# Kernel tuning notes

Hardware: AMD Instinct MI355X
Metric: run time of the kernel (lower is better)

The kernel has to match this reference:

```python
import jax, jax.numpy as jnp
import numpy as np

NUM_HEADS = 16
NUM_KV_HEADS = 4
HEAD_DIM = 128
SCALE = 0.08838834764831845  # 1/sqrt(128)
BATCH = 4
SEQLEN = 1024
TOTAL = BATCH * SEQLEN


def setup_inputs() -> dict:
    key = jax.random.key(0)
    kq, kk, kv = jax.random.split(key, 3)
    q = jax.random.normal(kq, (TOTAL, NUM_HEADS, HEAD_DIM), dtype=jnp.float32)
    k = jax.random.normal(kk, (TOTAL, NUM_KV_HEADS, HEAD_DIM), dtype=jnp.float32)
    v = jax.random.normal(kv, (TOTAL, NUM_KV_HEADS, HEAD_DIM), dtype=jnp.float32)
    cu = jnp.arange(BATCH + 1, dtype=jnp.int32) * SEQLEN  # [0,1024,2048,3072,4096]
    return {"q": q, "k": k, "v": v, "cu_seqlens_q": cu, "cu_seqlens_k": cu}


def reference(q, k, v, cu_seqlens_q, cu_seqlens_k):
    # Prefill varlen causal attention (block_tables=None, empty kv cache).
    # Equal-length segments -> reshape packed tokens to [B, S, H, D].
    B = cu_seqlens_q.shape[0] - 1
    S = q.shape[0] // B
    H, Dh = q.shape[1], q.shape[2]
    Hkv = k.shape[1]
    g = H // Hkv  # GQA group size

    qb = q.reshape(B, S, H, Dh)
    # repeat_interleave kv heads to match query heads
    kb = jnp.repeat(k.reshape(B, S, Hkv, Dh), g, axis=2)  # [B,S,H,Dh]
    vb = jnp.repeat(v.reshape(B, S, Hkv, Dh), g, axis=2)

    scores = jnp.einsum('bqhd,bkhd->bhqk', qb, kb) * SCALE  # [B,H,S,S]
    causal = jnp.tril(jnp.ones((S, S), dtype=bool))
    scores = jnp.where(causal, scores, jnp.finfo(scores.dtype).min)
    probs = jax.nn.softmax(scores, axis=-1)
    o = jnp.einsum('bhqk,bkhd->bqhd', probs, vb)  # [B,S,H,Dh]
    return o.reshape(B * S, H, Dh)
```

## Files before the change

kernel.cpp:

```cpp
#include <hip/hip_runtime.h>
#include <cstddef>

#define NH 16
#define NKV 4
#define HD 128
#define SEQ 1024
#define SCALE_F 0.08838834764831845f

typedef __attribute__((ext_vector_type(8))) short short8;
typedef __attribute__((ext_vector_type(4))) float floatx4;

union F8 { short8 v; unsigned short u[8]; };

__device__ __forceinline__ unsigned short f2bf(float f) {
  unsigned int u = __float_as_uint(f);
  u += 0x7FFFu + ((u >> 16) & 1u);
  return (unsigned short)(u >> 16);
}

__device__ __forceinline__ void glds16(const void* g, void* l) {
  __builtin_amdgcn_global_load_lds(
      (const __attribute__((address_space(1))) unsigned int*)g,
      (__attribute__((address_space(3))) unsigned int*)l, 16, 0, 0);
}

__global__ __launch_bounds__(256) void prepass(const float* __restrict__ kg,
                                               const float* __restrict__ vg,
                                               unsigned short* __restrict__ Ktg,
                                               unsigned short* __restrict__ Vtg) {
  __shared__ float Vl[32 * 132];
  const int tid = threadIdx.x;
  const int bid = blockIdx.x;
  if (bid < 512) {
    const int bkvh = bid >> 5, tile = bid & 31;
    const int b = bkvh >> 2, kvh = bkvh & 3;
    const int kpos = tid >> 3;
    const int d8base = (tid & 7) * 2;
    const size_t tok = (size_t)b * SEQ + tile * 32 + kpos;
    const float* src = kg + (tok * NKV + kvh) * HD + d8base * 8;
    unsigned short* dstT = Ktg + (size_t)bid * 4096;
#pragma unroll
    for (int i = 0; i < 2; ++i) {
      floatx4 a = ((const floatx4*)src)[0];
      floatx4 c = ((const floatx4*)src)[1];
      F8 t;
#pragma unroll
      for (int j = 0; j < 4; ++j) { t.u[j] = f2bf(a[j]); t.u[4 + j] = f2bf(c[j]); }
      const int blk = kpos * 16 + ((d8base + i) ^ (kpos & 15));
      *(short8*)(dstT + blk * 8) = t.v;
      src += 8;
    }
  } else {
    const int bb = bid - 512;
    const int bkvh = bb >> 5, tile = bb & 31;
    const int b = bkvh >> 2, kvh = bkvh & 3;
    const int r = tid >> 3;
    const int c16 = (tid & 7) * 16;
    const size_t tok = (size_t)b * SEQ + tile * 32 + r;
    const float* src = vg + (tok * NKV + kvh) * HD + c16;
#pragma unroll
    for (int j = 0; j < 4; ++j)
      *(floatx4*)&Vl[r * 132 + c16 + j * 4] = ((const floatx4*)src)[j];
    __syncthreads();
    unsigned short* dstT = Vtg + (size_t)bb * 4096;
#pragma unroll
    for (int i = 0; i < 2; ++i) {
      const int o = tid * 2 + i;
      const int d = o >> 2, s8 = o & 3;
      F8 t;
#pragma unroll
      for (int j = 0; j < 8; ++j) {
        const int s = s8 * 8 + j;
        const int k = (s >> 1) + ((s & 1) << 4);
        t.u[j] = f2bf(Vl[k * 132 + d]);
      }
      const int blk = d * 4 + (s8 ^ (d & 3));
      *(short8*)(dstT + blk * 8) = t.v;
    }
  }
}

__global__ __launch_bounds__(256, 4)
void fa_fwd2(const float* __restrict__ qg, const unsigned short* __restrict__ Ktg,
             const unsigned short* __restrict__ Vtg, float* __restrict__ og) {
  __shared__ __align__(16) unsigned short Kb[2][4096];
  __shared__ __align__(16) unsigned short Vb[2][4096];
  __shared__ __align__(16) unsigned int Pb[4][16 * 20];

  const int tid = threadIdx.x;
  const int wave = tid >> 6;
  const int lane = tid & 63;
  const int col = lane & 15;
  const int quad = lane >> 4;

  const int idx = blockIdx.x;
  const int g = idx >> 8;
  const int u = (idx >> 6) & 3;
  const int bh = idx & 63;
  const int qt = g * 4 + ((u + g) & 3);
  const int h = bh & 15;
  const int b = bh >> 4;
  const int kvh = h >> 2;
  const int seg = b * SEQ;
  const int wq0 = qt * 64 + wave * 16;
  const int tb = (b * NKV + kvh) * 32;

  F8 qf[4];
  {
    const float* qp = qg + ((size_t)(seg + wq0 + col) * NH + h) * HD + quad * 8;
#pragma unroll
    for (int ks = 0; ks < 4; ++ks) {
      floatx4 a = ((const floatx4*)(qp + ks * 32))[0];
      floatx4 c = ((const floatx4*)(qp + ks * 32))[1];
#pragma unroll
      for (int j = 0; j < 4; ++j) {
        qf[ks].u[j] = f2bf(a[j] * SCALE_F);
        qf[ks].u[4 + j] = f2bf(c[j] * SCALE_F);
      }
    }
  }

  floatx4 acc[8];
#pragma unroll
  for (int dt = 0; dt < 8; ++dt) acc[dt] = (floatx4){0.f, 0.f, 0.f, 0.f};
  float lsum[4] = {0.f, 0.f, 0.f, 0.f};

  const int nkt = 2 * (qt + 1);
  const int stoff = wave * 2048 + lane * 16;

  {
    const char* gK = (const char*)Ktg + (size_t)tb * 8192 + stoff;
    char* lK = (char*)&Kb[0][0] + wave * 2048;
    glds16(gK, lK);
    glds16(gK + 1024, lK + 1024);
    const char* gV = (const char*)Vtg + (size_t)tb * 8192 + stoff;
    char* lV = (char*)&Vb[0][0] + wave * 2048;
    glds16(gV, lV);
    glds16(gV + 1024, lV + 1024);
  }
  __syncthreads();

  for (int kt = 0; kt < nkt; ++kt) {
    const int cb = kt & 1, nb = cb ^ 1;
    if (kt + 1 < nkt) {
      const char* gK = (const char*)Ktg + (size_t)(tb + kt + 1) * 8192 + stoff;
      char* lK = (char*)&Kb[nb][0] + wave * 2048;
      glds16(gK, lK);
      glds16(gK + 1024, lK + 1024);
      const char* gV = (const char*)Vtg + (size_t)(tb + kt + 1) * 8192 + stoff;
      char* lV = (char*)&Vb[nb][0] + wave * 2048;
      glds16(gV, lV);
      glds16(gV + 1024, lV + 1024);
    }
    const int kbase = kt * 32;
    if (kbase <= wq0 + 15) {
      floatx4 s0 = {0.f, 0.f, 0.f, 0.f}, s1 = {0.f, 0.f, 0.f, 0.f};
#pragma unroll
      for (int ks = 0; ks < 4; ++ks) {
        F8 k0, k1;
        k0.v = *(const short8*)&Kb[cb][(col * 16 + ((ks * 4 + quad) ^ col)) * 8];
        k1.v = *(const short8*)&Kb[cb][((16 + col) * 16 + ((ks * 4 + quad) ^ col)) * 8];
        s0 = __builtin_amdgcn_mfma_f32_16x16x32_bf16(qf[ks].v, k0.v, s0, 0, 0, 0);
        s1 = __builtin_amdgcn_mfma_f32_16x16x32_bf16(qf[ks].v, k1.v, s1, 0, 0, 0);
      }
      const bool diag = (kbase + 31 > wq0);
#pragma unroll
      for (int r = 0; r < 4; ++r) {
        float p0 = __expf(s0[r]);
        float p1 = __expf(s1[r]);
        if (diag) {
          const int q0 = wq0 + quad * 4 + r;
          p0 = (kbase + col > q0) ? 0.f : p0;
          p1 = (kbase + 16 + col > q0) ? 0.f : p1;
        }
        lsum[r] += p0 + p1;
        Pb[wave][(quad * 4 + r) * 20 + col] =
            (unsigned int)f2bf(p0) | ((unsigned int)f2bf(p1) << 16);
      }
      F8 pa;
      pa.v = *(const short8*)&Pb[wave][col * 20 + quad * 4];
#pragma unroll
      for (int dt = 0; dt < 8; ++dt) {
        F8 vb;
        vb.v = *(const short8*)&Vb[cb][((dt * 16 + col) * 4 + (quad ^ (col & 3))) * 8];
        acc[dt] = __builtin_amdgcn_mfma_f32_16x16x32_bf16(pa.v, vb.v, acc[dt], 0, 0, 0);
      }
    }
    __syncthreads();
  }

#pragma unroll
  for (int r = 0; r < 4; ++r) {
    float l = lsum[r];
    l += __shfl_xor(l, 1);
    l += __shfl_xor(l, 2);
    l += __shfl_xor(l, 4);
    l += __shfl_xor(l, 8);
    const float inv = 1.0f / l;
    float* op = og + ((size_t)(seg + wq0 + quad * 4 + r) * NH + h) * HD;
#pragma unroll
    for (int dt = 0; dt < 8; ++dt) op[dt * 16 + col] = acc[dt][r] * inv;
  }
}

#define KST 136
#define VST 40
#define PST 40

__global__ __launch_bounds__(256, 2)
void fa_fwd(const float* __restrict__ qg, const float* __restrict__ kg,
            const float* __restrict__ vg, float* __restrict__ og) {
  __shared__ unsigned short Klds[32 * KST];
  __shared__ unsigned short Vt[HD * VST];
  __shared__ unsigned short Pl[4][32 * PST];

  const int tid = threadIdx.x;
  const int wave = tid >> 6;
  const int lane = tid & 63;
  const int col = lane & 15;
  const int quad = lane >> 4;

  const int idx = blockIdx.x;
  const int raw = idx & 7;
  const int qt = (idx & 256) ? raw : 7 - raw;
  const int bh = idx >> 3;
  const int h = bh & 15;
  const int b = bh >> 4;
  const int kvh = h >> 2;
  const int seg = b * SEQ;
  const int wq0 = qt * 128 + wave * 32;

  F8 qf[2][4];
#pragma unroll
  for (int mt = 0; mt < 2; ++mt) {
    const size_t qrow = (size_t)(seg + wq0 + mt * 16 + col);
    const float* qp = qg + (qrow * NH + h) * HD + quad * 8;
#pragma unroll
    for (int ks = 0; ks < 4; ++ks) {
      const floatx4* p4 = (const floatx4*)(qp + ks * 32);
      floatx4 a = p4[0], c = p4[1];
#pragma unroll
      for (int j = 0; j < 4; ++j) {
        qf[mt][ks].u[j] = f2bf(a[j] * SCALE_F);
        qf[mt][ks].u[4 + j] = f2bf(c[j] * SCALE_F);
      }
    }
  }

  floatx4 acc[2][8];
#pragma unroll
  for (int mt = 0; mt < 2; ++mt)
#pragma unroll
    for (int dt = 0; dt < 8; ++dt)
      acc[mt][dt] = (floatx4){0.f, 0.f, 0.f, 0.f};
  float lsum[2][4];
#pragma unroll
  for (int mt = 0; mt < 2; ++mt)
#pragma unroll
    for (int r = 0; r < 4; ++r) lsum[mt][r] = 0.f;

  const int nkt = 4 * (qt + 1);
  const int sr = tid >> 3;
  const int sc = (tid & 7) * 16;

  for (int kt = 0; kt < nkt; ++kt) {
    const int kbase = kt * 32;
    __syncthreads();
    {
      const size_t tok = (size_t)(seg + kbase + sr);
      const floatx4* kp4 = (const floatx4*)(kg + (tok * NKV + kvh) * HD + sc);
      floatx4 kv0 = kp4[0], kv1 = kp4[1], kv2 = kp4[2], kv3 = kp4[3];
      float kf32[16] = {kv0[0],kv0[1],kv0[2],kv0[3], kv1[0],kv1[1],kv1[2],kv1[3],
                        kv2[0],kv2[1],kv2[2],kv2[3], kv3[0],kv3[1],kv3[2],kv3[3]};
      unsigned int* dst = (unsigned int*)&Klds[sr * KST + sc];
#pragma unroll
      for (int j = 0; j < 8; ++j)
        dst[j] = (unsigned int)f2bf(kf32[2 * j]) | ((unsigned int)f2bf(kf32[2 * j + 1]) << 16);
      const floatx4* vp4 = (const floatx4*)(vg + (tok * NKV + kvh) * HD + sc);
      floatx4 vv0 = vp4[0], vv1 = vp4[1], vv2 = vp4[2], vv3 = vp4[3];
      unsigned short vb[16] = {
        f2bf(vv0[0]),f2bf(vv0[1]),f2bf(vv0[2]),f2bf(vv0[3]),
        f2bf(vv1[0]),f2bf(vv1[1]),f2bf(vv1[2]),f2bf(vv1[3]),
        f2bf(vv2[0]),f2bf(vv2[1]),f2bf(vv2[2]),f2bf(vv2[3]),
        f2bf(vv3[0]),f2bf(vv3[1]),f2bf(vv3[2]),f2bf(vv3[3])};
#pragma unroll
      for (int s = 0; s < 16; ++s) {
        int j = (s + tid) & 15;
        Vt[(sc + j) * VST + sr] = vb[j];
      }
    }
    __syncthreads();

    if (kbase > wq0 + 31) continue;

    F8 kf[4][2];
#pragma unroll
    for (int ks = 0; ks < 4; ++ks)
#pragma unroll
      for (int nt = 0; nt < 2; ++nt)
        kf[ks][nt].v = *(const short8*)&Klds[(nt * 16 + col) * KST + ks * 32 + quad * 8];

#pragma unroll
    for (int mt = 0; mt < 2; ++mt) {
      floatx4 s0 = {0.f, 0.f, 0.f, 0.f}, s1 = {0.f, 0.f, 0.f, 0.f};
#pragma unroll
      for (int ks = 0; ks < 4; ++ks) {
        s0 = __builtin_amdgcn_mfma_f32_16x16x32_bf16(qf[mt][ks].v, kf[ks][0].v, s0, 0, 0, 0);
        s1 = __builtin_amdgcn_mfma_f32_16x16x32_bf16(qf[mt][ks].v, kf[ks][1].v, s1, 0, 0, 0);
      }
      const int q0 = wq0 + mt * 16 + quad * 4;
      const bool diag = (kbase + 31 > wq0 + mt * 16);
      unsigned short* pw = &Pl[wave][(mt * 16 + quad * 4) * PST];
#pragma unroll
      for (int r = 0; r < 4; ++r) {
        float p0 = __expf(s0[r]);
        float p1 = __expf(s1[r]);
        if (diag) {
          p0 = (kbase + col > q0 + r) ? 0.f : p0;
          p1 = (kbase + 16 + col > q0 + r) ? 0.f : p1;
        }
        lsum[mt][r] += p0 + p1;
        pw[r * PST + col] = f2bf(p0);
        pw[r * PST + 16 + col] = f2bf(p1);
      }
    }
    F8 pa[2];
#pragma unroll
    for (int mt = 0; mt < 2; ++mt)
      pa[mt].v = *(const short8*)&Pl[wave][(mt * 16 + col) * PST + quad * 8];
#pragma unroll
    for (int dt = 0; dt < 8; ++dt) {
      F8 vb;
      vb.v = *(const short8*)&Vt[(dt * 16 + col) * VST + quad * 8];
#pragma unroll
      for (int mt = 0; mt < 2; ++mt)
        acc[mt][dt] = __builtin_amdgcn_mfma_f32_16x16x32_bf16(pa[mt].v, vb.v, acc[mt][dt], 0, 0, 0);
    }
  }

#pragma unroll
  for (int mt = 0; mt < 2; ++mt) {
#pragma unroll
    for (int r = 0; r < 4; ++r) {
      float l = lsum[mt][r];
      l += __shfl_xor(l, 1);
      l += __shfl_xor(l, 2);
      l += __shfl_xor(l, 4);
      l += __shfl_xor(l, 8);
      const float inv = 1.0f / l;
      const int qi = wq0 + mt * 16 + quad * 4 + r;
      float* op = og + ((size_t)(seg + qi) * NH + h) * HD;
#pragma unroll
      for (int dt = 0; dt < 8; ++dt)
        op[dt * 16 + col] = acc[mt][dt][r] * inv;
    }
  }
}

extern "C" void kernel_launch(void* const* d_in, const int* in_sizes, int n_in,
                              void* d_out, int out_size, void* d_ws, size_t ws_size,
                              hipStream_t stream) {
  const float* q = (const float*)d_in[0];
  const float* k = (const float*)d_in[1];
  const float* v = (const float*)d_in[2];
  float* out = (float*)d_out;
  if (ws_size >= (size_t)(8 * 1024 * 1024)) {
    unsigned short* Ktg = (unsigned short*)d_ws;
    unsigned short* Vtg = Ktg + 2097152;
    hipLaunchKernelGGL(prepass, dim3(1024), dim3(256), 0, stream, k, v, Ktg, Vtg);
    hipLaunchKernelGGL(fa_fwd2, dim3(1024), dim3(256), 0, stream, q, Ktg, Vtg, out);
  } else {
    hipLaunchKernelGGL(fa_fwd, dim3(512), dim3(256), 0, stream, q, k, v, out);
  }
}
```

Before: 130.9 us.

## Read V directly from global, use exp2 with prescaled Q, packed bf16 convert

Removes the LDS staging buffer for V and loads V fragments straight from the pre-transposed global workspace inside the PV loop, halving LDS traffic and async copies. Folds log2(e) into the Q scale so softmax uses the native exp2 instruction. Replaces manual bf16 rounding of P with the hardware packed convert. Direct global V loads add latency on the MFMA path and repeat reads across waves, relying on cache hits.

```diff
diff --git a/kernel.cpp b/kernel.cpp
--- a/kernel.cpp
+++ b/kernel.cpp
@@ -6,6 +6,7 @@
 #define HD 128
 #define SEQ 1024
 #define SCALE_F 0.08838834764831845f
+#define QSCALE 0.12751743f
 
 typedef __attribute__((ext_vector_type(8))) short short8;
 typedef __attribute__((ext_vector_type(4))) float floatx4;
@@ -16,6 +17,12 @@
   unsigned int u = __float_as_uint(f);
   u += 0x7FFFu + ((u >> 16) & 1u);
   return (unsigned short)(u >> 16);
+}
+
+__device__ __forceinline__ unsigned int pk_bf16(float lo, float hi) {
+  unsigned int r;
+  asm("v_cvt_pk_bf16_f32 %0, %1, %2" : "=v"(r) : "v"(lo), "v"(hi));
+  return r;
 }
 
 __device__ __forceinline__ void glds16(const void* g, void* l) {
@@ -81,10 +88,9 @@
 }
 
 __global__ __launch_bounds__(256, 4)
-void fa_fwd2(const float* __restrict__ qg, const unsigned short* __restrict__ Ktg,
+void fa_fwd6(const float* __restrict__ qg, const unsigned short* __restrict__ Ktg,
              const unsigned short* __restrict__ Vtg, float* __restrict__ og) {
   __shared__ __align__(16) unsigned short Kb[2][4096];
-  __shared__ __align__(16) unsigned short Vb[2][4096];
   __shared__ __align__(16) unsigned int Pb[4][16 * 20];
 
   const int tid = threadIdx.x;
@@ -114,8 +120,8 @@
       floatx4 c = ((const floatx4*)(qp + ks * 32))[1];
 #pragma unroll
       for (int j = 0; j < 4; ++j) {
-        qf[ks].u[j] = f2bf(a[j] * SCALE_F);
-        qf[ks].u[4 + j] = f2bf(c[j] * SCALE_F);
+        qf[ks].u[j] = f2bf(a[j] * QSCALE);
+        qf[ks].u[4 + j] = f2bf(c[j] * QSCALE);
       }
     }
   }
@@ -133,10 +139,6 @@
     char* lK = (char*)&Kb[0][0] + wave * 2048;
     glds16(gK, lK);
     glds16(gK + 1024, lK + 1024);
-    const char* gV = (const char*)Vtg + (size_t)tb * 8192 + stoff;
-    char* lV = (char*)&Vb[0][0] + wave * 2048;
-    glds16(gV, lV);
-    glds16(gV + 1024, lV + 1024);
   }
   __syncthreads();
 
@@ -147,10 +149,6 @@
       char* lK = (char*)&Kb[nb][0] + wave * 2048;
       glds16(gK, lK);
       glds16(gK + 1024, lK + 1024);
-      const char* gV = (const char*)Vtg + (size_t)(tb + kt + 1) * 8192 + stoff;
-      char* lV = (char*)&Vb[nb][0] + wave * 2048;
-      glds16(gV, lV);
-      glds16(gV + 1024, lV + 1024);
     }
     const int kbase = kt * 32;
     if (kbase <= wq0 + 15) {
@@ -166,23 +164,23 @@
       const bool diag = (kbase + 31 > wq0);
 #pragma unroll
       for (int r = 0; r < 4; ++r) {
-        float p0 = __expf(s0[r]);
-        float p1 = __expf(s1[r]);
+        float p0 = __builtin_amdgcn_exp2f(s0[r]);
+        float p1 = __builtin_amdgcn_exp2f(s1[r]);
         if (diag) {
           const int q0 = wq0 + quad * 4 + r;
           p0 = (kbase + col > q0) ? 0.f : p0;
           p1 = (kbase + 16 + col > q0) ? 0.f : p1;
         }
         lsum[r] += p0 + p1;
-        Pb[wave][(quad * 4 + r) * 20 + col] =
-            (unsigned int)f2bf(p0) | ((unsigned int)f2bf(p1) << 16);
+        Pb[wave][(quad * 4 + r) * 20 + col] = pk_bf16(p0, p1);
       }
       F8 pa;
       pa.v = *(const short8*)&Pb[wave][col * 20 + quad * 4];
+      const unsigned short* Vt = Vtg + (size_t)(tb + kt) * 4096;
 #pragma unroll
       for (int dt = 0; dt < 8; ++dt) {
         F8 vb;
-        vb.v = *(const short8*)&Vb[cb][((dt * 16 + col) * 4 + (quad ^ (col & 3))) * 8];
+        vb.v = *(const short8*)&Vt[((dt * 16 + col) * 4 + (quad ^ (col & 3))) * 8];
         acc[dt] = __builtin_amdgcn_mfma_f32_16x16x32_bf16(pa.v, vb.v, acc[dt], 0, 0, 0);
       }
     }
@@ -368,7 +366,7 @@
     unsigned short* Ktg = (unsigned short*)d_ws;
     unsigned short* Vtg = Ktg + 2097152;
     hipLaunchKernelGGL(prepass, dim3(1024), dim3(256), 0, stream, k, v, Ktg, Vtg);
-    hipLaunchKernelGGL(fa_fwd2, dim3(1024), dim3(256), 0, stream, q, Ktg, Vtg, out);
+    hipLaunchKernelGGL(fa_fwd6, dim3(1024), dim3(256), 0, stream, q, Ktg, Vtg, out);
   } else {
     hipLaunchKernelGGL(fa_fwd, dim3(512), dim3(256), 0, stream, q, k, v, out);
   }
```

After: 140.5 us. 7.4% more time.
